# Performance work log

Measured on AMD Instinct MI355X. Metric: run time of the kernel, lower is better.

Reference implementation:

```python
import jax, jax.numpy as jnp
import numpy as np

HIDDEN = 2048
FFN = 8192
NUM_EXPERTS = 8
TOP_K = 2


def setup_inputs() -> dict:
    key = jax.random.key(0)
    ks = jax.random.split(key, 6)
    scale_h = 1.0 / np.sqrt(HIDDEN)
    scale_f = 1.0 / np.sqrt(FFN)
    return {
        "hidden_states": jax.random.normal(ks[0], (4, 2048, HIDDEN), jnp.float32),
        "gate_w": jax.random.normal(ks[1], (NUM_EXPERTS, HIDDEN), jnp.float32) * scale_h,
        "w1": jax.random.normal(ks[2], (NUM_EXPERTS, HIDDEN, FFN), jnp.float32) * scale_h,
        "b1": jax.random.normal(ks[3], (NUM_EXPERTS, FFN), jnp.float32) * 0.01,
        "w2": jax.random.normal(ks[4], (NUM_EXPERTS, FFN, HIDDEN), jnp.float32) * scale_f,
        "b2": jax.random.normal(ks[5], (NUM_EXPERTS, HIDDEN), jnp.float32) * 0.01,
    }


def reference(hidden_states, gate_w, w1, b1, w2, b2):
    B, S, H = hidden_states.shape
    E = gate_w.shape[0]
    tokens = hidden_states.reshape(-1, H)  # [T, H]

    # Router: softmax gate, top-2, renormalize selected weights
    logits = tokens @ gate_w.T  # [T, E]
    probs = jax.nn.softmax(logits, axis=-1)
    topk_w, topk_idx = jax.lax.top_k(probs, TOP_K)  # [T, 2]
    topk_w = topk_w / jnp.sum(topk_w, axis=-1, keepdims=True)

    # Dense combine weights: w_dense[t, e] = routing weight of token t for expert e
    w_dense = jnp.sum(jax.nn.one_hot(topk_idx, E, dtype=topk_w.dtype) * topk_w[..., None], axis=1)  # [T, E]

    # Per-expert FFN (exact GELU as nn.GELU default), weighted scatter-combine
    combined = jnp.zeros_like(tokens)
    for e in range(E):  # small fixed expert count
        h = jax.nn.gelu(tokens @ w1[e] + b1[e], approximate=False)  # [T, F]
        combined = combined + w_dense[:, e:e + 1] * (h @ w2[e] + b2[e])

    return combined.reshape(B, S, H) + hidden_states
```

## Files before the change

kernel.cpp:

```cpp
#include <hip/hip_runtime.h>
#include <hip/hip_bf16.h>

#define T_TOK 8192
#define HID 2048
#define FFN_ 8192
#define NE 8
#define MAXR 18432

typedef __attribute__((ext_vector_type(8))) short bf16x8;
typedef __attribute__((ext_vector_type(4))) float f32x4;
typedef __attribute__((ext_vector_type(8))) unsigned short u16x8;

__device__ __forceinline__ unsigned short f2bf(float f) {
  unsigned int u = __float_as_uint(f);
  u += 0x7fffu + ((u >> 16) & 1u);
  return (unsigned short)(u >> 16);
}
__device__ __forceinline__ float bf2f(unsigned short h) {
  return __uint_as_float(((unsigned int)h) << 16);
}

__device__ __forceinline__ void gload_lds16(const ushort* g, ushort* l) {
  __builtin_amdgcn_global_load_lds(
      (const __attribute__((address_space(1))) unsigned int*)g,
      (__attribute__((address_space(3))) unsigned int*)l, 16, 0, 0);
}

__device__ __forceinline__ float gelu_f(float v) {
  float u = v * (0.7978845608f + 0.0356774081f * v * v);
  float a = fabsf(u);
  float ex = __expf(-2.f * a);
  float r = 1.f / (1.f + ex);
  float th = (1.f - ex) * r;
  th = (u >= 0.f) ? th : -th;
  return 0.5f * v * (1.f + th);
}

__global__ __launch_bounds__(256) void router_kernel(
    const float* __restrict__ x, const float* __restrict__ gw,
    int* __restrict__ topk_idx, float* __restrict__ topk_w, int* __restrict__ counts)
{
  int lane = threadIdx.x & 63;
  int w = threadIdx.x >> 6;
  int t = blockIdx.x * 4 + w;
  const float* xr = x + (size_t)t * HID;
  float acc[NE];
#pragma unroll
  for (int e = 0; e < NE; ++e) acc[e] = 0.f;
  for (int h = lane; h < HID; h += 64) {
    float xv = xr[h];
#pragma unroll
    for (int e = 0; e < NE; ++e) acc[e] = fmaf(xv, gw[e * HID + h], acc[e]);
  }
#pragma unroll
  for (int e = 0; e < NE; ++e) {
#pragma unroll
    for (int s = 32; s > 0; s >>= 1) acc[e] += __shfl_xor(acc[e], s);
  }
  if (lane == 0) {
    int i0 = 0; float v0 = acc[0];
#pragma unroll
    for (int e = 1; e < NE; ++e) { if (acc[e] > v0) { v0 = acc[e]; i0 = e; } }
    int i1 = -1; float v1 = -3.4e38f;
#pragma unroll
    for (int e = 0; e < NE; ++e) { if (e != i0 && acc[e] > v1) { v1 = acc[e]; i1 = e; } }
    float r = __expf(v1 - v0);
    float w0 = 1.f / (1.f + r);
    float w1 = r * w0;
    topk_idx[2 * t] = i0; topk_idx[2 * t + 1] = i1;
    topk_w[2 * t] = w0;   topk_w[2 * t + 1] = w1;
    atomicAdd(&counts[i0], 1);
    atomicAdd(&counts[i1], 1);
  }
}

__global__ void offsets_kernel(const int* __restrict__ counts, int* __restrict__ offs) {
  if (threadIdx.x == 0 && blockIdx.x == 0) {
    int o = 0;
#pragma unroll
    for (int e = 0; e < NE; ++e) { offs[e] = o; o += (counts[e] + 255) & ~255; }
    offs[NE] = o;
  }
}

__global__ __launch_bounds__(256) void scatter_kernel(
    const int* __restrict__ topk_idx, const float* __restrict__ topk_w,
    const int* __restrict__ offs, int* __restrict__ cursors,
    int* __restrict__ slot_token, float* __restrict__ slot_w, int* __restrict__ token_slot)
{
  int t = blockIdx.x * blockDim.x + threadIdx.x;
  if (t >= T_TOK) return;
#pragma unroll
  for (int k = 0; k < 2; ++k) {
    int e = topk_idx[2 * t + k];
    int pos = atomicAdd(&cursors[e], 1);
    int slot = offs[e] + pos;
    slot_token[slot] = t;
    slot_w[slot] = topk_w[2 * t + k];
    token_slot[2 * t + k] = slot;
  }
}

__device__ __forceinline__ void wconv_body(
    ushort* ldsbuf, const float* __restrict__ src0, ushort* __restrict__ dst0,
    int R, int C, int b)
{
  ushort (*tile)[524] = (ushort (*)[524])ldsbuf;
  const int spr = C >> 9;
  const int spe = (R >> 6) * spr;
  const int e = b / spe;
  const int s = b - e * spe;
  const int r0 = (s / spr) << 6;
  const int c0 = (s - (s / spr) * spr) << 9;
  const float* src = src0 + (size_t)e * R * C;
  ushort* dst = dst0 + (size_t)e * R * C;
  const int t = threadIdx.x;

#pragma unroll
  for (int i = 0; i < 16; ++i) {
    int idx = (i << 9) + t;
    int row = idx >> 7;
    int c4 = (idx & 127) << 2;
    float4 v = *(const float4*)&src[(size_t)(r0 + row) * C + c0 + c4];
    ushort4 u;
    u.x = f2bf(v.x); u.y = f2bf(v.y); u.z = f2bf(v.z); u.w = f2bf(v.w);
    *(ushort4*)&tile[row][c4] = u;
  }
  __syncthreads();
#pragma unroll
  for (int i = 0; i < 8; ++i) {
    int idx = (i << 9) + t;
    int c = idx >> 3;
    int r8 = (idx & 7) << 3;
    u16x8 o;
#pragma unroll
    for (int j = 0; j < 8; ++j) o[j] = tile[r8 + j][c];
    *(u16x8*)&dst[(size_t)(c0 + c) * R + r0 + r8] = o;
  }
}

__global__ __launch_bounds__(512) void wconvert_kernel(
    const float* __restrict__ src0, ushort* __restrict__ dst0, int R, int C)
{
  __shared__ ushort lds[64 * 524];
  wconv_body(lds, src0, dst0, R, C, blockIdx.x);
}

__device__ __forceinline__ void gather_body(
    const float* __restrict__ x, const int* __restrict__ slot_token,
    ushort* __restrict__ Xg, int b)
{
  int row = b * 2 + (threadIdx.x >> 8);
  int tok = slot_token[row];
  int c = (threadIdx.x & 255) * 8;
  ushort* dst = Xg + (size_t)row * HID + c;
  if (tok < 0) {
    u16x8 z = {0, 0, 0, 0, 0, 0, 0, 0};
    *(u16x8*)dst = z;
  } else {
    const float* s = x + (size_t)tok * HID + c;
    float4 a = *(const float4*)s;
    float4 bb = *(const float4*)(s + 4);
    u16x8 v;
    v[0] = f2bf(a.x); v[1] = f2bf(a.y); v[2] = f2bf(a.z); v[3] = f2bf(a.w);
    v[4] = f2bf(bb.x); v[5] = f2bf(bb.y); v[6] = f2bf(bb.z); v[7] = f2bf(bb.w);
    *(u16x8*)dst = v;
  }
}

__global__ __launch_bounds__(512) void gather_kernel512(
    const float* __restrict__ x, const int* __restrict__ slot_token, ushort* __restrict__ Xg)
{
  gather_body(x, slot_token, Xg, blockIdx.x);
}

__global__ __launch_bounds__(512) void gather_conv_kernel(
    const float* __restrict__ w1, ushort* __restrict__ w1t,
    const float* __restrict__ x, const int* __restrict__ slot_token,
    ushort* __restrict__ Xg, int convBlocks)
{
  __shared__ ushort lds[64 * 524];
  int b = blockIdx.x;
  if (b < convBlocks)
    wconv_body(lds, w1, w1t, HID, FFN_, b);
  else
    gather_body(x, slot_token, Xg, b - convBlocks);
}


#define VMWG() do { if constexpr (TM == 256) asm volatile("s_waitcnt vmcnt(6)" ::: "memory"); \
                    else                     asm volatile("s_waitcnt vmcnt(5)" ::: "memory"); } while (0)
#define VMW0() do { asm volatile("s_waitcnt vmcnt(0)" ::: "memory"); } while (0)
#define SCB()  __builtin_amdgcn_sched_barrier(0)
#define BAR()  __builtin_amdgcn_s_barrier()

#define STG_A(BUF, HALF, T) do {                                            \
    ushort* _d = lds + (BUF) * BUFS + (HALF) * REGA + tid * 8;              \
    gload_lds16(sA0 + (size_t)(HALF) * HOFFA + (size_t)(T) * 64, _d);       \
    if constexpr (TM == 256)                                                \
      gload_lds16(sA1 + (size_t)(HALF) * HOFFA + (size_t)(T) * 64, _d + 4096); \
  } while (0)
#define STG_B(BUF, HALF, T) do {                                            \
    ushort* _d = lds + (BUF) * BUFS + 2 * REGA + (HALF) * 8192 + tid * 8;   \
    gload_lds16(sB0 + (size_t)(HALF) * 32 * K + (size_t)(T) * 64, _d);      \
    gload_lds16(sB1 + (size_t)(HALF) * 32 * K + (size_t)(T) * 64, _d + 4096); \
  } while (0)

#define LDA(BUF, MQ) do {                                                   \
    _Pragma("unroll") for (int mm = 0; mm < MA; ++mm) {                     \
      const ushort* _p = lds + (BUF) * BUFS + (MQ) * REGA + aoff + mm * 1024; \
      af[mm][0] = *(const bf16x8*)(_p + ck0);                               \
      af[mm][1] = *(const bf16x8*)(_p + ck1);                               \
    } } while (0)
#define LDB(BUF, NQ) do {                                                   \
    _Pragma("unroll") for (int nn = 0; nn < 2; ++nn) {                      \
      const ushort* _p = lds + (BUF) * BUFS + 2 * REGA + (NQ) * 8192 + boff + nn * 1024; \
      bf[NQ][nn][0] = *(const bf16x8*)(_p + ck0);                           \
      bf[NQ][nn][1] = *(const bf16x8*)(_p + ck1);                           \
    } } while (0)

#define MM(MQ, NQ) do {                                                     \
    __builtin_amdgcn_s_setprio(1);                                          \
    _Pragma("unroll") for (int mm = 0; mm < MA; ++mm)                       \
    _Pragma("unroll") for (int nn = 0; nn < 2; ++nn) {                      \
      acc[(MQ)*MA+mm][(NQ)*2+nn] = __builtin_amdgcn_mfma_f32_16x16x32_bf16( \
          af[mm][0], bf[NQ][nn][0], acc[(MQ)*MA+mm][(NQ)*2+nn], 0, 0, 0);   \
      acc[(MQ)*MA+mm][(NQ)*2+nn] = __builtin_amdgcn_mfma_f32_16x16x32_bf16( \
          af[mm][1], bf[NQ][nn][1], acc[(MQ)*MA+mm][(NQ)*2+nn], 0, 0, 0);   \
    }                                                                       \
    __builtin_amdgcn_s_setprio(0);                                          \
  } while (0)

template <int EPI, int TM>
__device__ __forceinline__ void gemm_body(
    ushort* lds,
    const ushort* __restrict__ A, const ushort* __restrict__ Bt,
    const float* __restrict__ bias, ushort* __restrict__ Cout,
    const float* __restrict__ slot_w, const int* __restrict__ offs,
    int K, int N, int gy, int nwg, int bidx)
{
  constexpr int REGA = TM * 32;
  constexpr int BUFS = 2 * REGA + 16384;
  constexpr int MA = TM / 64;
  constexpr int HOFFA_ROWS = TM / 4;

  const int tid = threadIdx.x;
  const size_t HOFFA = (size_t)HOFFA_ROWS * K;
  int wg = bidx;
  int cpx = nwg >> 3;
  wg = (wg & 7) * cpx + (wg >> 3);
  int cb = wg / gy;
  int rb = wg - cb * gy;

  int total = offs[NE];
  int row0 = rb * TM;
  if (row0 >= total) return;
  int e = 0;
#pragma unroll
  for (int i = 1; i < NE; ++i) e += (row0 >= offs[i]) ? 1 : 0;

  const ushort* Ag = A + (size_t)row0 * K;
  const ushort* Bg = Bt + ((size_t)e * N + (size_t)cb * 256) * K;

  const int pr0 = tid >> 3;
  const int pr1 = 64 + pr0;
  const int j0 = (tid & 7) ^ (pr0 & 7);
  const int j1 = (tid & 7) ^ (pr1 & 7);
  const int rA0 = (TM == 256) ? pr0 : (((pr0 >> 5) << 6) + (pr0 & 31));
  const int rA1 = 128 + pr0;
  const int rB0 = ((pr0 >> 5) << 6) + (pr0 & 31);
  const int rB1 = ((pr1 >> 5) << 6) + (pr1 & 31);
  const ushort* sA0 = Ag + (size_t)rA0 * K + j0 * 8;
  const ushort* sA1 = Ag + (size_t)rA1 * K + j1 * 8;
  const ushort* sB0 = Bg + (size_t)rB0 * K + j0 * 8;
  const ushort* sB1 = Bg + (size_t)rB1 * K + j1 * 8;

  const int lane = tid & 63;
  const int wid = tid >> 6;
  const int wr = wid >> 2, wc = wid & 3;
  const int lrow = lane & 15, g = lane >> 4, x7 = lrow & 7;
  const int ck0 = (g ^ x7) * 8;
  const int ck1 = ((4 + g) ^ x7) * 8;
  const int aoff = (wr * (TM / 4) + lrow) * 64;
  const int boff = (wc * 32 + lrow) * 64;

  f32x4 acc[TM / 32][4] = {};
  bf16x8 af[MA][2], bf[2][2][2];

  const int NT = K >> 6;
  const int NITER = NT >> 1;

  STG_A(0, 0, 0); STG_A(0, 1, 0); STG_B(0, 0, 0); STG_B(0, 1, 0);
  STG_A(1, 0, 1); STG_B(1, 0, 1); STG_B(1, 1, 1);
  VMWG();
  BAR(); SCB();

  for (int it = 0; it < NITER; ++it) {
    const int tb = 2 * it + 1;
    const int tn0 = 2 * it + 2;
    const int tn1 = 2 * it + 3;
    const bool more0 = tn0 < NT;
    const bool more1 = tn1 < NT;
    const bool last = (it + 1 == NITER);

    STG_A(1, 1, tb);
    LDA(0, 0); LDB(0, 0);
    LDB(0, 1);
    MM(0, 0);
    MM(0, 1);
    BAR(); SCB();

    if (more0) { STG_A(0, 0, tn0); STG_B(0, 0, tn0); }
    LDA(0, 1);
    MM(1, 0);
    if (more0) STG_B(0, 1, tn0);
    MM(1, 1);
    if (last) { VMW0(); } else { VMWG(); }
    BAR(); SCB();

    if (more0) STG_A(0, 1, tn0);
    LDA(1, 0); LDB(1, 0);
    LDB(1, 1);
    MM(0, 0);
    MM(0, 1);
    BAR(); SCB();

    if (more1) { STG_A(1, 0, tn1); STG_B(1, 0, tn1); }
    LDA(1, 1);
    MM(1, 0);
    if (more1) STG_B(1, 1, tn1);
    MM(1, 1);
    if (more1) VMWG();
    BAR(); SCB();
  }

  const int colb = cb * 256 + wc * 64;
  const int rowb = row0 + wr * (TM / 2);
  float bv[4];
#pragma unroll
  for (int n = 0; n < 4; ++n)
    bv[n] = bias[(size_t)e * N + colb + n * 16 + lrow];
#pragma unroll
  for (int m = 0; m < TM / 32; ++m) {
    const int mq = m / MA, mm = m % MA;
    const int gr = rowb + mq * (TM / 4) + mm * 16 + g * 4;
#pragma unroll
    for (int i = 0; i < 4; ++i) {
      const int grow = gr + i;
      float sw = (EPI == 1) ? slot_w[grow] : 0.f;
      ushort* crow = Cout + (size_t)grow * N + colb + lrow;
#pragma unroll
      for (int n = 0; n < 4; ++n) {
        float v = acc[m][n][i] + bv[n];
        if (EPI == 0) v = gelu_f(v);
        else          v *= sw;
        crow[n * 16] = f2bf(v);
      }
    }
  }
}

template <int EPI, int TM>
__global__ __launch_bounds__(512, 2) void gemm256_kernel(
    const ushort* __restrict__ A, const ushort* __restrict__ Bt,
    const float* __restrict__ bias, ushort* __restrict__ Cout,
    const float* __restrict__ slot_w, const int* __restrict__ offs,
    int K, int N, int gy)
{
  __shared__ ushort lds[TM * 128 + 32768];
  gemm_body<EPI, TM>(lds, A, Bt, bias, Cout, slot_w, offs, K, N, gy,
                     (int)gridDim.x, (int)blockIdx.x);
}

__global__ __launch_bounds__(512, 2) void gemm1_conv_kernel(
    const ushort* __restrict__ A, const ushort* __restrict__ Bt,
    const float* __restrict__ bias, ushort* __restrict__ Cout,
    const int* __restrict__ offs,
    const float* __restrict__ w2, ushort* __restrict__ w2t, int gemmBlocks)
{
  __shared__ ushort lds[65536];
  if ((int)blockIdx.x < gemmBlocks)
    gemm_body<0, 256>(lds, A, Bt, bias, Cout, nullptr, offs, HID, FFN_,
                      MAXR / 256, gemmBlocks, (int)blockIdx.x);
  else
    wconv_body(lds, w2, w2t, FFN_, HID, (int)blockIdx.x - gemmBlocks);
}

__global__ __launch_bounds__(256) void combine_kernel(
    const float* __restrict__ x, const ushort* __restrict__ Yp,
    const int* __restrict__ token_slot, float* __restrict__ out)
{
  int t = blockIdx.x;
  int s0 = token_slot[2 * t], s1 = token_slot[2 * t + 1];
  int c = threadIdx.x * 8;
  const float* xr = x + (size_t)t * HID + c;
  u16x8 y0 = *(const u16x8*)&Yp[(size_t)s0 * HID + c];
  u16x8 y1 = *(const u16x8*)&Yp[(size_t)s1 * HID + c];
  float4 xa = *(const float4*)xr;
  float4 xb = *(const float4*)(xr + 4);
  float4 oa, ob;
  oa.x = xa.x + bf2f(y0[0]) + bf2f(y1[0]);
  oa.y = xa.y + bf2f(y0[1]) + bf2f(y1[1]);
  oa.z = xa.z + bf2f(y0[2]) + bf2f(y1[2]);
  oa.w = xa.w + bf2f(y0[3]) + bf2f(y1[3]);
  ob.x = xb.x + bf2f(y0[4]) + bf2f(y1[4]);
  ob.y = xb.y + bf2f(y0[5]) + bf2f(y1[5]);
  ob.z = xb.z + bf2f(y0[6]) + bf2f(y1[6]);
  ob.w = xb.w + bf2f(y0[7]) + bf2f(y1[7]);
  float* orow = out + (size_t)t * HID + c;
  *(float4*)orow = oa;
  *(float4*)(orow + 4) = ob;
}

extern "C" void kernel_launch(void* const* d_in, const int* in_sizes, int n_in,
                              void* d_out, int out_size, void* d_ws, size_t ws_size,
                              hipStream_t stream)
{
  const float* x  = (const float*)d_in[0];
  const float* gw = (const float*)d_in[1];
  const float* w1 = (const float*)d_in[2];
  const float* b1 = (const float*)d_in[3];
  const float* w2 = (const float*)d_in[4];
  const float* b2 = (const float*)d_in[5];
  float* out = (float*)d_out;

  char* ws = (char*)d_ws;
  ushort* wT  = (ushort*)(ws + 0);
  ushort* Hb  = (ushort*)(ws + 268435456);
  ushort* Xg  = (ushort*)(ws + 570425344);
  ushort* Yp  = Xg;
  char* sm = ws + 645922816;
  int*   slot_token = (int*)(sm);
  float* slot_w     = (float*)(sm + 73728);
  int*   token_slot = (int*)(sm + 147456);
  int*   topk_idx   = (int*)(sm + 212992);
  float* topk_w     = (float*)(sm + 278528);
  int*   counts     = (int*)(sm + 344064);
  int*   cursors    = (int*)(sm + 344096);
  int*   offs       = (int*)(sm + 344128);

  const size_t W2T_OFF = 646267136ULL;
  const bool fused = ws_size >= W2T_OFF + 268435456ULL;
  ushort* w2t = fused ? (ushort*)(ws + W2T_OFF) : wT;

  hipMemsetAsync(counts, 0, 64, stream);
  hipMemsetAsync(slot_token, 0xFF, MAXR * 4, stream);

  router_kernel<<<dim3(T_TOK / 4), dim3(256), 0, stream>>>(x, gw, topk_idx, topk_w, counts);
  offsets_kernel<<<dim3(1), dim3(64), 0, stream>>>(counts, offs);
  scatter_kernel<<<dim3(T_TOK / 256), dim3(256), 0, stream>>>(
      topk_idx, topk_w, offs, cursors, slot_token, slot_w, token_slot);

  gather_conv_kernel<<<dim3(4096 + MAXR / 2), dim3(512), 0, stream>>>(
      w1, wT, x, slot_token, Xg, 4096);

  if (fused) {
    gemm1_conv_kernel<<<dim3(2304 + 4096), dim3(512), 0, stream>>>(
        Xg, wT, b1, Hb, offs, w2, w2t, 2304);
  } else {
    gemm256_kernel<0, 256><<<dim3(2304), dim3(512), 0, stream>>>(
        Xg, wT, b1, Hb, nullptr, offs, HID, FFN_, MAXR / 256);
    wconvert_kernel<<<dim3(4096), dim3(512), 0, stream>>>(w2, wT, FFN_, HID);
  }

  gemm256_kernel<1, 128><<<dim3(1152), dim3(512), 0, stream>>>(
      Hb, w2t, b2, Yp, slot_w, offs, FFN_, HID, MAXR / 128);

  combine_kernel<<<dim3(T_TOK), dim3(256), 0, stream>>>(x, Yp, token_slot, out);
}
```

Baseline: 1.822 ms.

## Add triple-buffered 128x256 GEMM2 kernel with deeper prefetch pipeline

Replaces the second expert GEMM launch with a dedicated kernel using three LDS buffers, prefetching two K-tiles ahead and interleaving staging with MFMA quadrants. The intent is to hide global-to-LDS latency better during the long K=8192 reduction. It uses more LDS per block (about 144KB), which may limit occupancy to fewer blocks per CU than the launch bounds request. It also removes an unused gather kernel.

```diff
diff --git a/kernel.cpp b/kernel.cpp
--- a/kernel.cpp
+++ b/kernel.cpp
@@ -168,12 +168,6 @@
   }
 }
 
-__global__ __launch_bounds__(512) void gather_kernel512(
-    const float* __restrict__ x, const int* __restrict__ slot_token, ushort* __restrict__ Xg)
-{
-  gather_body(x, slot_token, Xg, blockIdx.x);
-}
-
 __global__ __launch_bounds__(512) void gather_conv_kernel(
     const float* __restrict__ w1, ushort* __restrict__ w1t,
     const float* __restrict__ x, const int* __restrict__ slot_token,
@@ -191,6 +185,7 @@
 #define VMWG() do { if constexpr (TM == 256) asm volatile("s_waitcnt vmcnt(6)" ::: "memory"); \
                     else                     asm volatile("s_waitcnt vmcnt(5)" ::: "memory"); } while (0)
 #define VMW0() do { asm volatile("s_waitcnt vmcnt(0)" ::: "memory"); } while (0)
+#define VMW6() do { asm volatile("s_waitcnt vmcnt(6)" ::: "memory"); } while (0)
 #define SCB()  __builtin_amdgcn_sched_barrier(0)
 #define BAR()  __builtin_amdgcn_s_barrier()
 
@@ -384,6 +379,147 @@
                       MAXR / 256, gemmBlocks, (int)blockIdx.x);
   else
     wconv_body(lds, w2, w2t, FFN_, HID, (int)blockIdx.x - gemmBlocks);
+}
+
+
+#define T3_STG_A(BASE, HALF, T) \
+    gload_lds16(sA0 + (size_t)(HALF) * HOFF3 + (size_t)(T) * 64, (BASE) + (HALF) * 4096 + tid * 8)
+#define T3_STG_B(BASE, HALF, T) do {                                        \
+    ushort* _d = (BASE) + 8192 + (HALF) * 8192 + tid * 8;                   \
+    gload_lds16(sB0 + (size_t)(HALF) * 32 * K3 + (size_t)(T) * 64, _d);     \
+    gload_lds16(sB1 + (size_t)(HALF) * 32 * K3 + (size_t)(T) * 64, _d + 4096); \
+  } while (0)
+#define T3_LDA(BASE, MQ) do {                                               \
+    _Pragma("unroll") for (int mm = 0; mm < 2; ++mm) {                      \
+      const ushort* _p = (BASE) + (MQ) * 4096 + aoff + mm * 1024;           \
+      af[mm][0] = *(const bf16x8*)(_p + ck0);                               \
+      af[mm][1] = *(const bf16x8*)(_p + ck1);                               \
+    } } while (0)
+#define T3_LDB(BASE, NQ) do {                                               \
+    _Pragma("unroll") for (int nn = 0; nn < 2; ++nn) {                      \
+      const ushort* _p = (BASE) + 8192 + (NQ) * 8192 + boff + nn * 1024;    \
+      bf[NQ][nn][0] = *(const bf16x8*)(_p + ck0);                           \
+      bf[NQ][nn][1] = *(const bf16x8*)(_p + ck1);                           \
+    } } while (0)
+#define T3_MM(MQ, NQ) do {                                                  \
+    __builtin_amdgcn_s_setprio(1);                                          \
+    _Pragma("unroll") for (int mm = 0; mm < 2; ++mm)                        \
+    _Pragma("unroll") for (int nn = 0; nn < 2; ++nn) {                      \
+      acc[(MQ)*2+mm][(NQ)*2+nn] = __builtin_amdgcn_mfma_f32_16x16x32_bf16(  \
+          af[mm][0], bf[NQ][nn][0], acc[(MQ)*2+mm][(NQ)*2+nn], 0, 0, 0);    \
+      acc[(MQ)*2+mm][(NQ)*2+nn] = __builtin_amdgcn_mfma_f32_16x16x32_bf16(  \
+          af[mm][1], bf[NQ][nn][1], acc[(MQ)*2+mm][(NQ)*2+nn], 0, 0, 0);    \
+    }                                                                       \
+    __builtin_amdgcn_s_setprio(0);                                          \
+  } while (0)
+
+__global__ __launch_bounds__(512, 2) void gemm2_tri_kernel(
+    const ushort* __restrict__ A, const ushort* __restrict__ Bt,
+    const float* __restrict__ bias, ushort* __restrict__ Cout,
+    const float* __restrict__ slot_w, const int* __restrict__ offs, int gy)
+{
+  constexpr int K3 = FFN_;
+  constexpr int N3 = HID;
+  __shared__ ushort lds[73728];
+
+  const int tid = threadIdx.x;
+  int nwg = gridDim.x;
+  int wg = blockIdx.x;
+  int cpx = nwg >> 3;
+  wg = (wg & 7) * cpx + (wg >> 3);
+  int cb = wg / gy;
+  int rb = wg - cb * gy;
+
+  int total = offs[NE];
+  int row0 = rb * 128;
+  if (row0 >= total) return;
+  int e = 0;
+#pragma unroll
+  for (int i = 1; i < NE; ++i) e += (row0 >= offs[i]) ? 1 : 0;
+
+  const ushort* Ag = A + (size_t)row0 * K3;
+  const ushort* Bg = Bt + ((size_t)e * N3 + (size_t)cb * 256) * K3;
+
+  const size_t HOFF3 = (size_t)32 * K3;
+  const int pr0 = tid >> 3;
+  const int pr1 = 64 + pr0;
+  const int j0 = (tid & 7) ^ (pr0 & 7);
+  const int j1 = (tid & 7) ^ (pr1 & 7);
+  const int rA0 = ((pr0 >> 5) << 6) + (pr0 & 31);
+  const int rB0 = ((pr0 >> 5) << 6) + (pr0 & 31);
+  const int rB1 = ((pr1 >> 5) << 6) + (pr1 & 31);
+  const ushort* sA0 = Ag + (size_t)rA0 * K3 + j0 * 8;
+  const ushort* sB0 = Bg + (size_t)rB0 * K3 + j0 * 8;
+  const ushort* sB1 = Bg + (size_t)rB1 * K3 + j1 * 8;
+
+  const int lane = tid & 63;
+  const int wid = tid >> 6;
+  const int wr = wid >> 2, wc = wid & 3;
+  const int lrow = lane & 15, g = lane >> 4, x7 = lrow & 7;
+  const int ck0 = (g ^ x7) * 8;
+  const int ck1 = ((4 + g) ^ x7) * 8;
+  const int aoff = (wr * 32 + lrow) * 64;
+  const int boff = (wc * 32 + lrow) * 64;
+
+  f32x4 acc[4][4] = {};
+  bf16x8 af[2][2], bf[2][2][2];
+
+  constexpr int NT = K3 >> 6;
+
+  {
+    ushort* b0 = lds;
+    ushort* b1 = lds + 24576;
+    T3_STG_A(b0, 0, 0); T3_STG_A(b0, 1, 0); T3_STG_B(b0, 0, 0); T3_STG_B(b0, 1, 0);
+    T3_STG_A(b1, 0, 1); T3_STG_A(b1, 1, 1); T3_STG_B(b1, 0, 1); T3_STG_B(b1, 1, 1);
+  }
+  VMW6();
+  BAR(); SCB();
+
+  int br = 0, bw = 2;
+  for (int t = 0; t < NT; ++t) {
+    ushort* Rb = lds + br * 24576;
+    ushort* Wb = lds + bw * 24576;
+    const bool stg = (t + 2 < NT);
+
+    if (stg) { T3_STG_A(Wb, 0, t + 2); T3_STG_A(Wb, 1, t + 2); }
+    T3_LDA(Rb, 0); T3_LDB(Rb, 0);
+    T3_MM(0, 0);
+    if (stg) T3_STG_B(Wb, 0, t + 2);
+    T3_LDB(Rb, 1);
+    T3_MM(0, 1);
+    if (stg) T3_STG_B(Wb, 1, t + 2);
+    T3_LDA(Rb, 1);
+    T3_MM(1, 0);
+    T3_MM(1, 1);
+    if (stg) { VMW6(); } else { VMW0(); }
+    BAR(); SCB();
+
+    br = (br == 2) ? 0 : br + 1;
+    bw = (bw == 2) ? 0 : bw + 1;
+  }
+
+  const int colb = cb * 256 + wc * 64;
+  const int rowb = row0 + wr * 64;
+  float bv[4];
+#pragma unroll
+  for (int n = 0; n < 4; ++n)
+    bv[n] = bias[(size_t)e * N3 + colb + n * 16 + lrow];
+#pragma unroll
+  for (int m = 0; m < 4; ++m) {
+    const int mq = m >> 1, mm = m & 1;
+    const int gr = rowb + mq * 32 + mm * 16 + g * 4;
+#pragma unroll
+    for (int i = 0; i < 4; ++i) {
+      const int grow = gr + i;
+      float sw = slot_w[grow];
+      ushort* crow = Cout + (size_t)grow * N3 + colb + lrow;
+#pragma unroll
+      for (int n = 0; n < 4; ++n) {
+        float v = (acc[m][n][i] + bv[n]) * sw;
+        crow[n * 16] = f2bf(v);
+      }
+    }
+  }
 }
 
 __global__ __launch_bounds__(256) void combine_kernel(
@@ -463,8 +599,8 @@
     wconvert_kernel<<<dim3(4096), dim3(512), 0, stream>>>(w2, wT, FFN_, HID);
   }
 
-  gemm256_kernel<1, 128><<<dim3(1152), dim3(512), 0, stream>>>(
-      Hb, w2t, b2, Yp, slot_w, offs, FFN_, HID, MAXR / 128);
+  gemm2_tri_kernel<<<dim3((HID / 256) * (MAXR / 128)), dim3(512), 0, stream>>>(
+      Hb, w2t, b2, Yp, slot_w, offs, MAXR / 128);
 
   combine_kernel<<<dim3(T_TOK), dim3(256), 0, stream>>>(x, Yp, token_slot, out);
 }
```

Measured after the change: 1.790 ms. Within noise of the previous version (-1.8%).
